# Optimization experiments

Hardware: AMD Instinct MI355X
Metric: run time of the kernel (lower is better)

Reference implementation:

```python
import jax, jax.numpy as jnp
import numpy as np

N_NODES = 50000
N_EDGES = 600000
EPS = 1e-5


def setup_inputs() -> dict:
    key = jax.random.key(0)
    ks = jax.random.split(key, 8)
    return {
        "x": jax.random.normal(ks[0], (N_NODES, 128), dtype=jnp.float32),
        "src": jax.random.randint(ks[1], (N_EDGES,), 0, N_NODES, dtype=jnp.int32),
        "dst": jax.random.randint(ks[2], (N_EDGES,), 0, N_NODES, dtype=jnp.int32),
        "weight": jax.random.uniform(ks[3], (N_EDGES,), dtype=jnp.float32),
        "W1": jax.random.normal(ks[4], (128, 128), dtype=jnp.float32) * 0.05,
        "b1": jnp.zeros((128,), dtype=jnp.float32),
        "gamma1": jnp.ones((128,), dtype=jnp.float32),
        "beta1": jnp.zeros((128,), dtype=jnp.float32),
        "W2": jax.random.normal(ks[5], (128, 64), dtype=jnp.float32) * 0.05,
        "b2": jnp.zeros((64,), dtype=jnp.float32),
        "gamma2": jnp.ones((64,), dtype=jnp.float32),
        "beta2": jnp.zeros((64,), dtype=jnp.float32),
        "W3": jax.random.normal(ks[6], (64, 32), dtype=jnp.float32) * 0.05,
        "b3": jnp.zeros((32,), dtype=jnp.float32),
    }


def _batchnorm(h, gamma, beta):
    # BatchNorm1d in training mode over the node axis (biased variance)
    mean = jnp.mean(h, axis=0)
    var = jnp.mean((h - mean) ** 2, axis=0)
    return gamma * (h - mean) * jax.lax.rsqrt(var + EPS) + beta


def reference(x, src, dst, weight, W1, b1, gamma1, beta1, W2, b2, gamma2, beta2, W3, b3):
    n = x.shape[0]
    # GCNConv: add self-loops with weight 1, symmetric normalization
    loop = jnp.arange(n, dtype=src.dtype)
    src_f = jnp.concatenate([src, loop])  # [E+N]
    dst_f = jnp.concatenate([dst, loop])
    w_f = jnp.concatenate([weight, jnp.ones((n,), dtype=weight.dtype)])
    deg = jax.ops.segment_sum(w_f, dst_f, num_segments=n)  # [N]
    dinv = jnp.where(deg > 0, deg ** -0.5, 0.0)
    norm = dinv[src_f] * w_f * dinv[dst_f]  # [E+N], same for every layer

    def conv(h, W, b):
        h = h @ W  # [N, out]
        msg = norm[:, None] * h[src_f]  # gather + edge scale
        return jax.ops.segment_sum(msg, dst_f, num_segments=n) + b

    h = conv(x, W1, b1)
    h = jax.nn.relu(_batchnorm(h, gamma1, beta1))
    h = conv(h, W2, b2)
    h = jax.nn.relu(_batchnorm(h, gamma2, beta2))
    h = conv(h, W3, b3)  # final BatchNorm is dropped by net[:-1] in encode()
    return h
```

## Files before the change

### kernel.cpp

```cpp
#include <hip/hip_runtime.h>
#include <hip/hip_bf16.h>

#define NN 50000
#define NE 600000
#define SLOTS 48

typedef unsigned short ushortT;
typedef unsigned int uintT;
typedef __attribute__((ext_vector_type(8))) short bf16x8;
typedef __attribute__((ext_vector_type(4))) float f32x4;

__device__ __forceinline__ ushortT f2bfbits(float f) {
    __hip_bfloat16 h = __float2bfloat16(f);
    return *reinterpret_cast<ushortT*>(&h);
}

__device__ __forceinline__ float4 unpack_bf4(uint2 p) {
    float4 r;
    r.x = __uint_as_float(p.x << 16);
    r.y = __uint_as_float(p.x & 0xffff0000u);
    r.z = __uint_as_float(p.y << 16);
    r.w = __uint_as_float(p.y & 0xffff0000u);
    return r;
}

__device__ __forceinline__ int esrc(uintT v) { return (int)(v & 0xFFFFu); }
__device__ __forceinline__ float ew(uintT v) { return __uint_as_float(v & 0xFFFF0000u); }

template <int K, int M>
__device__ __forceinline__ void pack_w_dev(const float* __restrict__ W,
                                           ushortT* __restrict__ Wp, int t) {
    constexpr int KC = K / 32;
    constexpr int CT = M / 16;
    if (t >= CT * KC * 64) return;
    int l = t & 63;
    int q = (t >> 6) % KC;
    int c = t / (64 * KC);
    int m = l & 15, quad = l >> 4;
    alignas(16) ushortT tmp[8];
#pragma unroll
    for (int j = 0; j < 8; ++j)
        tmp[j] = f2bfbits(W[(size_t)(q * 32 + quad * 8 + j) * M + c * 16 + m]);
    *reinterpret_cast<uint4*>(&Wp[(size_t)t * 8]) = *reinterpret_cast<const uint4*>(tmp);
}

__global__ void __launch_bounds__(256) prep_kernel(const float* __restrict__ W1,
                                                   const float* __restrict__ W2,
                                                   const float* __restrict__ W3,
                                                   ushortT* __restrict__ Wp1,
                                                   ushortT* __restrict__ Wp2,
                                                   ushortT* __restrict__ Wp3,
                                                   int* __restrict__ counts,
                                                   float* __restrict__ sums, int n) {
    int b = blockIdx.x, tid = threadIdx.x;
    if (b < 8) {
        pack_w_dev<128, 128>(W1, Wp1, b * 256 + tid);
    } else if (b < 12) {
        pack_w_dev<128, 64>(W2, Wp2, (b - 8) * 256 + tid);
    } else if (b < 13) {
        pack_w_dev<64, 32>(W3, Wp3, (b - 12) * 256 + tid);
    } else {
        int i = (b - 13) * 256 + tid;
        if (i < n) counts[i] = 0;
        if (b == 13) sums[tid] = 0.f;
    }
}

template <typename AT, int K, int M, bool FUSEBN>
__device__ __forceinline__ void gemm_dev(int bid, const AT* __restrict__ A,
                                         const ushortT* __restrict__ Wp,
                                         const float* __restrict__ sums,
                                         const float* __restrict__ gamma,
                                         const float* __restrict__ beta,
                                         ushortT* __restrict__ out, int N) {
    constexpr int KC = K / 32;
    constexpr int CT = M / 16;
    int wave = threadIdx.x >> 6;
    int lane = threadIdx.x & 63;
    int m = lane & 15, quad = lane >> 4;
    int rowbase = bid * 64 + wave * 16;
    int arow = min(rowbase + m, N - 1);

    f32x4 acc[CT] = {};
    const float invN = 1.0f / (float)N;

#pragma unroll
    for (int q = 0; q < KC; ++q) {
        int kb = q * 32 + quad * 8;
        float av[8];
        if constexpr (sizeof(AT) == 4) {
            const float* ap = (const float*)A + (size_t)arow * K + kb;
            float4 lo = *reinterpret_cast<const float4*>(ap);
            float4 hi = *reinterpret_cast<const float4*>(ap + 4);
            av[0] = lo.x; av[1] = lo.y; av[2] = lo.z; av[3] = lo.w;
            av[4] = hi.x; av[5] = hi.y; av[6] = hi.z; av[7] = hi.w;
        } else {
            const ushortT* ap = (const ushortT*)A + (size_t)arow * K + kb;
            uint4 p = *reinterpret_cast<const uint4*>(ap);
            float4 lo = unpack_bf4(make_uint2(p.x, p.y));
            float4 hi = unpack_bf4(make_uint2(p.z, p.w));
            av[0] = lo.x; av[1] = lo.y; av[2] = lo.z; av[3] = lo.w;
            av[4] = hi.x; av[5] = hi.y; av[6] = hi.z; av[7] = hi.w;
        }
        if constexpr (FUSEBN) {
#pragma unroll
            for (int j = 0; j < 8; ++j) {
                int k = kb + j;
                float mean = sums[k] * invN;
                float var = fmaf(-mean, mean, sums[K + k] * invN);
                var = var > 0.f ? var : 0.f;
                float sc = gamma[k] * rsqrtf(var + 1e-5f);
                float sh = fmaf(-mean, sc, beta[k]);
                av[j] = fmaxf(fmaf(av[j], sc, sh), 0.f);
            }
        }
        bf16x8 af;
#pragma unroll
        for (int j = 0; j < 8; ++j) af[j] = (short)f2bfbits(av[j]);
#pragma unroll
        for (int c = 0; c < CT; ++c) {
            bf16x8 bf = *reinterpret_cast<const bf16x8*>(
                &Wp[(((size_t)c * KC + q) * 64 + lane) * 8]);
            acc[c] = __builtin_amdgcn_mfma_f32_16x16x32_bf16(af, bf, acc[c], 0, 0, 0);
        }
    }
#pragma unroll
    for (int c = 0; c < CT; ++c) {
#pragma unroll
        for (int r = 0; r < 4; ++r) {
            int row = rowbase + quad * 4 + r;
            if (row < N) out[(size_t)row * M + c * 16 + m] = f2bfbits(acc[c][r]);
        }
    }
}

__global__ void __launch_bounds__(256) gemm1_fill_kernel(
    const float* __restrict__ x, const ushortT* __restrict__ Wp1,
    ushortT* __restrict__ hlin,
    const int* __restrict__ src, const int* __restrict__ dst, const float* __restrict__ w,
    int* __restrict__ counts, uintT* __restrict__ col_sw, int E, int N, int GB) {
    if ((int)blockIdx.x < GB) {
        gemm_dev<float, 128, 128, false>(blockIdx.x, x, Wp1, nullptr, nullptr, nullptr, hlin, N);
        return;
    }
    int e = ((int)blockIdx.x - GB) * 256 + threadIdx.x;
    if (e < E) {
        int d = dst[e];
        int pos = atomicAdd(&counts[d], 1);
        if (pos < SLOTS) {
            uintT rec = ((uintT)f2bfbits(w[e]) << 16) | (uintT)src[e];
            col_sw[(size_t)pos * N + d] = rec;
        }
    }
}

template <typename AT, int K, int M, bool FUSEBN>
__global__ void __launch_bounds__(256) mfma_gemm(const AT* __restrict__ A,
                                                 const ushortT* __restrict__ Wp,
                                                 const float* __restrict__ sums,
                                                 const float* __restrict__ gamma,
                                                 const float* __restrict__ beta,
                                                 ushortT* __restrict__ out, int N) {
    gemm_dev<AT, K, M, FUSEBN>(blockIdx.x, A, Wp, sums, gamma, beta, out, N);
}

__global__ void deg_dinv_kernel(const int* __restrict__ counts, const uintT* __restrict__ col_sw,
                                float* __restrict__ dinv, int n) {
    int i = blockIdx.x * 256 + threadIdx.x;
    if (i >= n) return;
    int c = min(counts[i], SLOTS);
    float s = 1.0f;
    for (int j = 0; j < c; ++j) s += ew(col_sw[(size_t)j * n + i]);
    dinv[i] = rsqrtf(s);
}

template <int C, bool OUTBF, bool ZERO>
__global__ void __launch_bounds__(256) csr_agg_kernel(const ushortT* __restrict__ hbf,
                                                      const int* __restrict__ counts,
                                                      const uintT* __restrict__ col_sw,
                                                      const float* __restrict__ dinv,
                                                      const float* __restrict__ bias,
                                                      void* __restrict__ out,
                                                      float* __restrict__ sums, int N) {
    if (ZERO && blockIdx.x == 0) sums[threadIdx.x] = 0.f;
    constexpr int C8 = C / 8;
    int idx = blockIdx.x * 256 + threadIdx.x;
    if (idx >= N * C8) return;
    int node = idx / C8;
    int c8 = idx - node * C8;
    const uint4* h8 = reinterpret_cast<const uint4*>(hbf);
    int cnt = min(counts[node], SLOTS);
    float di = dinv[node];
    float sl = di * di;
    uint4 hp = h8[idx];
    float4 hlo = unpack_bf4(make_uint2(hp.x, hp.y));
    float4 hhi = unpack_bf4(make_uint2(hp.z, hp.w));
    float4 blo = *reinterpret_cast<const float4*>(&bias[8 * c8]);
    float4 bhi = *reinterpret_cast<const float4*>(&bias[8 * c8 + 4]);
    float4 alo, ahi;
    alo.x = fmaf(sl, hlo.x, blo.x); alo.y = fmaf(sl, hlo.y, blo.y);
    alo.z = fmaf(sl, hlo.z, blo.z); alo.w = fmaf(sl, hlo.w, blo.w);
    ahi.x = fmaf(sl, hhi.x, bhi.x); ahi.y = fmaf(sl, hhi.y, bhi.y);
    ahi.z = fmaf(sl, hhi.z, bhi.z); ahi.w = fmaf(sl, hhi.w, bhi.w);
    const uintT* cs = col_sw + node;

#define ACC_EDGE(SW, DV)                                                \
    {                                                                   \
        float nrm = DV * ew(SW) * di;                                   \
        uint4 p = h8[(size_t)esrc(SW) * C8 + c8];                       \
        float4 lo = unpack_bf4(make_uint2(p.x, p.y));                   \
        float4 hi = unpack_bf4(make_uint2(p.z, p.w));                   \
        alo.x = fmaf(nrm, lo.x, alo.x); alo.y = fmaf(nrm, lo.y, alo.y); \
        alo.z = fmaf(nrm, lo.z, alo.z); alo.w = fmaf(nrm, lo.w, alo.w); \
        ahi.x = fmaf(nrm, hi.x, ahi.x); ahi.y = fmaf(nrm, hi.y, ahi.y); \
        ahi.z = fmaf(nrm, hi.z, ahi.z); ahi.w = fmaf(nrm, hi.w, ahi.w); \
    }

    int j = 0;
    for (; j + 4 <= cnt; j += 4) {
        uintT sw0 = cs[(size_t)(j + 0) * N];
        uintT sw1 = cs[(size_t)(j + 1) * N];
        uintT sw2 = cs[(size_t)(j + 2) * N];
        uintT sw3 = cs[(size_t)(j + 3) * N];
        float d0 = dinv[esrc(sw0)], d1 = dinv[esrc(sw1)];
        float d2 = dinv[esrc(sw2)], d3 = dinv[esrc(sw3)];
        ACC_EDGE(sw0, d0);
        ACC_EDGE(sw1, d1);
        ACC_EDGE(sw2, d2);
        ACC_EDGE(sw3, d3);
    }
    for (; j < cnt; ++j) {
        uintT sw = cs[(size_t)j * N];
        float dv = dinv[esrc(sw)];
        ACC_EDGE(sw, dv);
    }
#undef ACC_EDGE

    if constexpr (OUTBF) {
        alignas(16) ushortT tmp[8];
        tmp[0] = f2bfbits(alo.x); tmp[1] = f2bfbits(alo.y);
        tmp[2] = f2bfbits(alo.z); tmp[3] = f2bfbits(alo.w);
        tmp[4] = f2bfbits(ahi.x); tmp[5] = f2bfbits(ahi.y);
        tmp[6] = f2bfbits(ahi.z); tmp[7] = f2bfbits(ahi.w);
        reinterpret_cast<uint4*>(out)[idx] = *reinterpret_cast<const uint4*>(tmp);
    } else {
        float4* o4 = reinterpret_cast<float4*>(out);
        o4[idx * 2] = alo;
        o4[idx * 2 + 1] = ahi;
    }
}

#define BN_GRID 104
template <int C>
__global__ void __launch_bounds__(256) bn_stats_kernel(const ushortT* __restrict__ hbf,
                                                       float* __restrict__ sums, int N) {
    constexpr int C4 = C / 4;
    constexpr int SPB = 256 / C4;
    __shared__ float4 sm1[256], sm2[256];
    int tid = threadIdx.x;
    int c4 = tid % C4;
    int r0 = blockIdx.x * SPB + tid / C4;
    int stride = gridDim.x * SPB;
    const uint2* h2 = reinterpret_cast<const uint2*>(hbf);
    float4 s = make_float4(0.f, 0.f, 0.f, 0.f);
    float4 s2 = make_float4(0.f, 0.f, 0.f, 0.f);
    for (int r = r0; r < N; r += stride) {
        float4 v = unpack_bf4(h2[(size_t)r * C4 + c4]);
        s.x += v.x; s.y += v.y; s.z += v.z; s.w += v.w;
        s2.x = fmaf(v.x, v.x, s2.x);
        s2.y = fmaf(v.y, v.y, s2.y);
        s2.z = fmaf(v.z, v.z, s2.z);
        s2.w = fmaf(v.w, v.w, s2.w);
    }
    sm1[tid] = s; sm2[tid] = s2;
    __syncthreads();
#pragma unroll
    for (int off = 128; off >= C4; off >>= 1) {
        if (tid < off) {
            float4 a = sm1[tid + off], b = sm2[tid + off];
            float4 u = sm1[tid], v = sm2[tid];
            u.x += a.x; u.y += a.y; u.z += a.z; u.w += a.w;
            v.x += b.x; v.y += b.y; v.z += b.z; v.w += b.w;
            sm1[tid] = u; sm2[tid] = v;
        }
        __syncthreads();
    }
    if (tid < C4) {
        float4 a = sm1[tid], b = sm2[tid];
        unsafeAtomicAdd(&sums[4 * tid + 0], a.x);
        unsafeAtomicAdd(&sums[4 * tid + 1], a.y);
        unsafeAtomicAdd(&sums[4 * tid + 2], a.z);
        unsafeAtomicAdd(&sums[4 * tid + 3], a.w);
        unsafeAtomicAdd(&sums[C + 4 * tid + 0], b.x);
        unsafeAtomicAdd(&sums[C + 4 * tid + 1], b.y);
        unsafeAtomicAdd(&sums[C + 4 * tid + 2], b.z);
        unsafeAtomicAdd(&sums[C + 4 * tid + 3], b.w);
    }
}

extern "C" void kernel_launch(void* const* d_in, const int* in_sizes, int n_in,
                              void* d_out, int out_size, void* d_ws, size_t ws_size,
                              hipStream_t stream) {
    const float* x      = (const float*)d_in[0];
    const int*   src    = (const int*)d_in[1];
    const int*   dst    = (const int*)d_in[2];
    const float* weight = (const float*)d_in[3];
    const float* W1     = (const float*)d_in[4];
    const float* b1     = (const float*)d_in[5];
    const float* gamma1 = (const float*)d_in[6];
    const float* beta1  = (const float*)d_in[7];
    const float* W2     = (const float*)d_in[8];
    const float* b2     = (const float*)d_in[9];
    const float* gamma2 = (const float*)d_in[10];
    const float* beta2  = (const float*)d_in[11];
    const float* W3     = (const float*)d_in[12];
    const float* b3     = (const float*)d_in[13];
    float* out = (float*)d_out;

    const int N = NN, E = NE;

    char* ws = (char*)d_ws;
    size_t off = 0;
    auto alloc = [&](size_t bytes) {
        size_t r = off;
        off += (bytes + 255) & ~(size_t)255;
        return r;
    };
    float*   dinv    = (float*)(ws + alloc((size_t)N * 4));
    int*     counts  = (int*)(ws + alloc((size_t)N * 4));
    uintT*   col_sw  = (uintT*)(ws + alloc((size_t)N * SLOTS * 4));
    ushortT* hlin_bf = (ushortT*)(ws + alloc((size_t)N * 128 * 2));
    ushortT* hagg_bf = (ushortT*)(ws + alloc((size_t)N * 128 * 2));
    ushortT* Wp1     = (ushortT*)(ws + alloc(128 * 128 * 2));
    ushortT* Wp2     = (ushortT*)(ws + alloc(128 * 64 * 2));
    ushortT* Wp3     = (ushortT*)(ws + alloc(64 * 32 * 2));
    float*   sums    = (float*)(ws + alloc(256 * 4));

    dim3 blk(256);
    auto grd = [](long long n) { return dim3((unsigned)((n + 255) / 256)); };
    const int GB = (N + 63) / 64;
    const int DB = (N + 255) / 256;
    const int FB = (E + 255) / 256;

    prep_kernel<<<13 + DB, blk, 0, stream>>>(W1, W2, W3, Wp1, Wp2, Wp3, counts, sums, N);

    gemm1_fill_kernel<<<GB + FB, blk, 0, stream>>>(x, Wp1, hlin_bf,
                                                   src, dst, weight, counts, col_sw, E, N, GB);
    deg_dinv_kernel<<<DB, blk, 0, stream>>>(counts, col_sw, dinv, N);

    ushortT* h1agg = hagg_bf;
    csr_agg_kernel<128, true, false><<<grd((long long)N * 16), blk, 0, stream>>>(
        hlin_bf, counts, col_sw, dinv, b1, h1agg, sums, N);
    bn_stats_kernel<128><<<BN_GRID, 256, 0, stream>>>(h1agg, sums, N);

    ushortT* h2agg = hagg_bf;
    mfma_gemm<ushortT, 128, 64, true><<<GB, blk, 0, stream>>>(
        h1agg, Wp2, sums, gamma1, beta1, hlin_bf, N);
    csr_agg_kernel<64, true, true><<<grd((long long)N * 8), blk, 0, stream>>>(
        hlin_bf, counts, col_sw, dinv, b2, h2agg, sums, N);
    bn_stats_kernel<64><<<BN_GRID, 256, 0, stream>>>(h2agg, sums, N);

    mfma_gemm<ushortT, 64, 32, true><<<GB, blk, 0, stream>>>(
        h2agg, Wp3, sums, gamma2, beta2, hlin_bf, N);
    csr_agg_kernel<32, false, false><<<grd((long long)N * 4), blk, 0, stream>>>(
        hlin_bf, counts, col_sw, dinv, b3, out, sums, N);
}
```

Measured before the change: 261.5 us.

## Switch edge slots to node-major layout and precompute per-edge norms

Edge records move from a slot-major (pos*N+node) layout to a node-major (node*SLOTS+pos) layout, and deg_dinv reads them as uint4 vectors. A new norm_kernel precomputes each edge's symmetric normalization once, so the three aggregation passes no longer gather dinv[src]. The cost is an extra kernel and a second N*SLOTS float array. In the aggregation kernels, the threads that share a node now read the same contiguous row, while threads for different nodes stride by SLOTS*4 bytes, so coalescing changes rather than simply improving. The scattered writes in the fill phase also change pattern.

After: 271.6 us. 3.9% more time.

```diff
diff --git a/kernel.cpp b/kernel.cpp
--- a/kernel.cpp
+++ b/kernel.cpp
@@ -138,7 +138,7 @@
     const float* __restrict__ x, const ushortT* __restrict__ Wp1,
     ushortT* __restrict__ hlin,
     const int* __restrict__ src, const int* __restrict__ dst, const float* __restrict__ w,
-    int* __restrict__ counts, uintT* __restrict__ col_sw, int E, int N, int GB) {
+    int* __restrict__ counts, uintT* __restrict__ col_rec, int E, int N, int GB) {
     if ((int)blockIdx.x < GB) {
         gemm_dev<float, 128, 128, false>(blockIdx.x, x, Wp1, nullptr, nullptr, nullptr, hlin, N);
         return;
@@ -149,7 +149,7 @@
         int pos = atomicAdd(&counts[d], 1);
         if (pos < SLOTS) {
             uintT rec = ((uintT)f2bfbits(w[e]) << 16) | (uintT)src[e];
-            col_sw[(size_t)pos * N + d] = rec;
+            col_rec[(size_t)d * SLOTS + pos] = rec;
         }
     }
 }
@@ -164,20 +164,40 @@
     gemm_dev<AT, K, M, FUSEBN>(blockIdx.x, A, Wp, sums, gamma, beta, out, N);
 }
 
-__global__ void deg_dinv_kernel(const int* __restrict__ counts, const uintT* __restrict__ col_sw,
+__global__ void deg_dinv_kernel(const int* __restrict__ counts, const uintT* __restrict__ col_rec,
                                 float* __restrict__ dinv, int n) {
     int i = blockIdx.x * 256 + threadIdx.x;
     if (i >= n) return;
     int c = min(counts[i], SLOTS);
+    const uintT* cr = col_rec + (size_t)i * SLOTS;
     float s = 1.0f;
-    for (int j = 0; j < c; ++j) s += ew(col_sw[(size_t)j * n + i]);
+    int j = 0;
+    for (; j + 4 <= c; j += 4) {
+        uint4 p = *reinterpret_cast<const uint4*>(&cr[j]);
+        s += ew(p.x) + ew(p.y) + ew(p.z) + ew(p.w);
+    }
+    for (; j < c; ++j) s += ew(cr[j]);
     dinv[i] = rsqrtf(s);
+}
+
+__global__ void __launch_bounds__(256) norm_kernel(const int* __restrict__ counts,
+                                                   const uintT* __restrict__ col_rec,
+                                                   const float* __restrict__ dinv,
+                                                   float* __restrict__ col_nrm, int n) {
+    int idx = blockIdx.x * 256 + threadIdx.x;
+    if (idx >= n * SLOTS) return;
+    int node = idx / SLOTS;
+    int j = idx - node * SLOTS;
+    if (j >= min(counts[node], SLOTS)) return;
+    uintT rec = col_rec[idx];
+    col_nrm[idx] = dinv[node] * ew(rec) * dinv[esrc(rec)];
 }
 
 template <int C, bool OUTBF, bool ZERO>
 __global__ void __launch_bounds__(256) csr_agg_kernel(const ushortT* __restrict__ hbf,
                                                       const int* __restrict__ counts,
-                                                      const uintT* __restrict__ col_sw,
+                                                      const uintT* __restrict__ col_rec,
+                                                      const float* __restrict__ col_nrm,
                                                       const float* __restrict__ dinv,
                                                       const float* __restrict__ bias,
                                                       void* __restrict__ out,
@@ -202,37 +222,33 @@
     alo.z = fmaf(sl, hlo.z, blo.z); alo.w = fmaf(sl, hlo.w, blo.w);
     ahi.x = fmaf(sl, hhi.x, bhi.x); ahi.y = fmaf(sl, hhi.y, bhi.y);
     ahi.z = fmaf(sl, hhi.z, bhi.z); ahi.w = fmaf(sl, hhi.w, bhi.w);
-    const uintT* cs = col_sw + node;
-
-#define ACC_EDGE(SW, DV)                                                \
+    const uintT* cr = col_rec + (size_t)node * SLOTS;
+    const float* cn = col_nrm + (size_t)node * SLOTS;
+
+#define ACC_EDGE(RC, NRM)                                               \
     {                                                                   \
-        float nrm = DV * ew(SW) * di;                                   \
-        uint4 p = h8[(size_t)esrc(SW) * C8 + c8];                       \
+        uint4 p = h8[(size_t)esrc(RC) * C8 + c8];                       \
         float4 lo = unpack_bf4(make_uint2(p.x, p.y));                   \
         float4 hi = unpack_bf4(make_uint2(p.z, p.w));                   \
-        alo.x = fmaf(nrm, lo.x, alo.x); alo.y = fmaf(nrm, lo.y, alo.y); \
-        alo.z = fmaf(nrm, lo.z, alo.z); alo.w = fmaf(nrm, lo.w, alo.w); \
-        ahi.x = fmaf(nrm, hi.x, ahi.x); ahi.y = fmaf(nrm, hi.y, ahi.y); \
-        ahi.z = fmaf(nrm, hi.z, ahi.z); ahi.w = fmaf(nrm, hi.w, ahi.w); \
+        alo.x = fmaf(NRM, lo.x, alo.x); alo.y = fmaf(NRM, lo.y, alo.y); \
+        alo.z = fmaf(NRM, lo.z, alo.z); alo.w = fmaf(NRM, lo.w, alo.w); \
+        ahi.x = fmaf(NRM, hi.x, ahi.x); ahi.y = fmaf(NRM, hi.y, ahi.y); \
+        ahi.z = fmaf(NRM, hi.z, ahi.z); ahi.w = fmaf(NRM, hi.w, ahi.w); \
     }
 
     int j = 0;
     for (; j + 4 <= cnt; j += 4) {
-        uintT sw0 = cs[(size_t)(j + 0) * N];
-        uintT sw1 = cs[(size_t)(j + 1) * N];
-        uintT sw2 = cs[(size_t)(j + 2) * N];
-        uintT sw3 = cs[(size_t)(j + 3) * N];
-        float d0 = dinv[esrc(sw0)], d1 = dinv[esrc(sw1)];
-        float d2 = dinv[esrc(sw2)], d3 = dinv[esrc(sw3)];
-        ACC_EDGE(sw0, d0);
-        ACC_EDGE(sw1, d1);
-        ACC_EDGE(sw2, d2);
-        ACC_EDGE(sw3, d3);
+        uintT r0 = cr[j + 0], r1 = cr[j + 1], r2 = cr[j + 2], r3 = cr[j + 3];
+        float n0 = cn[j + 0], n1 = cn[j + 1], n2 = cn[j + 2], n3 = cn[j + 3];
+        ACC_EDGE(r0, n0);
+        ACC_EDGE(r1, n1);
+        ACC_EDGE(r2, n2);
+        ACC_EDGE(r3, n3);
     }
     for (; j < cnt; ++j) {
-        uintT sw = cs[(size_t)j * N];
-        float dv = dinv[esrc(sw)];
-        ACC_EDGE(sw, dv);
+        uintT rr = cr[j];
+        float nn = cn[j];
+        ACC_EDGE(rr, nn);
     }
 #undef ACC_EDGE
 
@@ -328,7 +344,8 @@
     };
     float*   dinv    = (float*)(ws + alloc((size_t)N * 4));
     int*     counts  = (int*)(ws + alloc((size_t)N * 4));
-    uintT*   col_sw  = (uintT*)(ws + alloc((size_t)N * SLOTS * 4));
+    uintT*   col_rec = (uintT*)(ws + alloc((size_t)N * SLOTS * 4));
+    float*   col_nrm = (float*)(ws + alloc((size_t)N * SLOTS * 4));
     ushortT* hlin_bf = (ushortT*)(ws + alloc((size_t)N * 128 * 2));
     ushortT* hagg_bf = (ushortT*)(ws + alloc((size_t)N * 128 * 2));
     ushortT* Wp1     = (ushortT*)(ws + alloc(128 * 128 * 2));
@@ -341,27 +358,29 @@
     const int GB = (N + 63) / 64;
     const int DB = (N + 255) / 256;
     const int FB = (E + 255) / 256;
+    const int NB = (N * SLOTS + 255) / 256;
 
     prep_kernel<<<13 + DB, blk, 0, stream>>>(W1, W2, W3, Wp1, Wp2, Wp3, counts, sums, N);
 
     gemm1_fill_kernel<<<GB + FB, blk, 0, stream>>>(x, Wp1, hlin_bf,
-                                                   src, dst, weight, counts, col_sw, E, N, GB);
-    deg_dinv_kernel<<<DB, blk, 0, stream>>>(counts, col_sw, dinv, N);
+                                                   src, dst, weight, counts, col_rec, E, N, GB);
+    deg_dinv_kernel<<<DB, blk, 0, stream>>>(counts, col_rec, dinv, N);
+    norm_kernel<<<NB, blk, 0, stream>>>(counts, col_rec, dinv, col_nrm, N);
 
     ushortT* h1agg = hagg_bf;
     csr_agg_kernel<128, true, false><<<grd((long long)N * 16), blk, 0, stream>>>(
-        hlin_bf, counts, col_sw, dinv, b1, h1agg, sums, N);
+        hlin_bf, counts, col_rec, col_nrm, dinv, b1, h1agg, sums, N);
     bn_stats_kernel<128><<<BN_GRID, 256, 0, stream>>>(h1agg, sums, N);
 
     ushortT* h2agg = hagg_bf;
     mfma_gemm<ushortT, 128, 64, true><<<GB, blk, 0, stream>>>(
         h1agg, Wp2, sums, gamma1, beta1, hlin_bf, N);
     csr_agg_kernel<64, true, true><<<grd((long long)N * 8), blk, 0, stream>>>(
-        hlin_bf, counts, col_sw, dinv, b2, h2agg, sums, N);
+        hlin_bf, counts, col_rec, col_nrm, dinv, b2, h2agg, sums, N);
     bn_stats_kernel<64><<<BN_GRID, 256, 0, stream>>>(h2agg, sums, N);
 
     mfma_gemm<ushortT, 64, 32, true><<<GB, blk, 0, stream>>>(
         h2agg, Wp3, sums, gamma2, beta2, hlin_bf, N);
     csr_agg_kernel<32, false, false><<<grd((long long)N * 4), blk, 0, stream>>>(
-        hlin_bf, counts, col_sw, dinv, b3, out, sums, N);
-}
+        hlin_bf, counts, col_rec, col_nrm, dinv, b3, out, sums, N);
+}
```
